# Performance work log

Hardware: AMD Instinct MI355X
Metric: run time of the kernel (lower is better)

The kernel has to match this reference:

```python
import jax, jax.numpy as jnp
import numpy as np

DIM = 256          # model dim
H = 8              # num heads
E = DIM // H       # head dim = 32
M = 32             # ball size
NB = 8192          # number of balls
N = NB * M         # total points = 262144
D3 = 3             # spatial dimensionality


def setup_inputs() -> dict:
    key = jax.random.key(0)
    ks = jax.random.split(key, 10)
    s = 1.0 / np.sqrt(DIM)
    return {
        "x": jax.random.normal(ks[0], (N, DIM), jnp.float32),
        "pos": jax.random.normal(ks[1], (N, D3), jnp.float32),
        "w_qkv": jax.random.normal(ks[2], (DIM, 3 * DIM), jnp.float32) * s,
        "b_qkv": jnp.zeros((3 * DIM,), jnp.float32),
        "w_pe": jax.random.normal(ks[3], (D3, DIM), jnp.float32) * (1.0 / np.sqrt(D3)),
        "b_pe": jnp.zeros((DIM,), jnp.float32),
        "w_proj": jax.random.normal(ks[4], (DIM, DIM), jnp.float32) * s,
        "b_proj": jnp.zeros((DIM,), jnp.float32),
        "sigma_att": -1.0 + 0.01 * jax.random.normal(ks[5], (1, H, 1, 1), jnp.float32),
    }


def reference(x, pos, w_qkv, b_qkv, w_pe, b_pe, w_proj, b_proj, sigma_att):
    n = x.shape[0] // M
    pos_b = pos.reshape(n, M, D3)                       # (n, m, 3)

    # eq. 9: relative position embedding wrt ball center
    centers = pos_b.mean(axis=1, keepdims=True)         # (n, 1, 3)
    rel = (pos_b - centers).reshape(n * M, D3)
    x = x + rel @ w_pe + b_pe                           # (N, DIM)

    # qkv projection; layout '(H E K)' with K fastest
    qkv = (x @ w_qkv + b_qkv).reshape(n, M, H, E, 3)
    q = jnp.transpose(qkv[..., 0], (0, 2, 1, 3))        # (n, H, m, E)
    k = jnp.transpose(qkv[..., 1], (0, 2, 1, 3))
    v = jnp.transpose(qkv[..., 2], (0, 2, 1, 3))

    # eq. 10: distance-based attention bias
    diff = pos_b[:, :, None, :] - pos_b[:, None, :, :]  # (n, m, m, 3)
    d2 = jnp.sum(diff * diff, axis=-1)
    dist = jnp.sqrt(jnp.maximum(d2, 1e-12))             # safe sqrt (grad at 0)
    bias = sigma_att * dist[:, None, :, :]              # (n, H, m, m)

    scale = 1.0 / np.sqrt(E)
    scores = jnp.einsum('nhme,nhke->nhmk', q, k) * scale + bias
    attn = jax.nn.softmax(scores, axis=-1)
    out = jnp.einsum('nhmk,nhke->nhme', attn, v)        # (n, H, m, E)
    out = jnp.transpose(out, (0, 2, 1, 3)).reshape(n * M, DIM)
    return out @ w_proj + b_proj
```

## Files before the change

kernel.cpp:

```cpp
#include <hip/hip_runtime.h>

#define NPTS   262144
#define NBALLS 8192
#define MSZ    32

typedef unsigned short u16;
typedef __attribute__((ext_vector_type(8))) unsigned short u16x8;
typedef __attribute__((ext_vector_type(8))) __bf16 bf16x8;
typedef __attribute__((ext_vector_type(4))) float f32x4;
typedef __attribute__((ext_vector_type(2))) unsigned u32x2;

__device__ inline u16 f2bf(float f) {
    unsigned u = __builtin_bit_cast(unsigned, f);
    u += 0x7fffu + ((u >> 16) & 1u);
    return (u16)(u >> 16);
}

__device__ inline unsigned pk2(float lo, float hi) {
    return (unsigned)f2bf(lo) | ((unsigned)f2bf(hi) << 16);
}

__device__ inline f32x4 mfma16(u16x8 a, u16x8 b, f32x4 c) {
    return __builtin_amdgcn_mfma_f32_16x16x32_bf16(
        __builtin_bit_cast(bf16x8, a), __builtin_bit_cast(bf16x8, b), c, 0, 0, 0);
}

__device__ inline void gload_lds16(const u16* g, u16* l) {
    __builtin_amdgcn_global_load_lds(
        (const __attribute__((address_space(1))) void*)g,
        (__attribute__((address_space(3))) void*)l, 16, 0, 0);
}

__global__ __launch_bounds__(256) void k0_wprep(const float* __restrict__ w_qkv,
                                                const float* __restrict__ b_qkv,
                                                const float* __restrict__ w_proj,
                                                u16* __restrict__ wqkvT2,
                                                u16* __restrict__ wpF,
                                                float* __restrict__ bq2) {
    int idx = blockIdx.x * 256 + threadIdx.x;
    if (idx < 768 * 256) {
        int cp = idx >> 8, r = idx & 255;
        int h = cp / 96, rem = cp % 96, mat = rem >> 5, e = rem & 31;
        int orig = h * 96 + e * 3 + mat;
        wqkvT2[cp * 256 + r] = f2bf(w_qkv[r * 768 + orig]);
        if (r == 0) bq2[cp] = b_qkv[orig];
    } else {
        int tid2 = idx - 768 * 256;
        int lane = tid2 & 63, ch = tid2 >> 6;
        int hk = ch & 7, gct = ch >> 3;
        int r15 = lane & 15, g4 = lane >> 4;
        u16x8 o;
#pragma unroll
        for (int j = 0; j < 8; ++j)
            o[j] = f2bf(w_proj[(size_t)(hk * 32 + g4 * 8 + j) * 256 + gct * 16 + r15]);
        *(u16x8*)&wpF[(size_t)tid2 * 8] = o;
    }
}

__global__ __launch_bounds__(512, 4) void k1_fused(const float* __restrict__ x,
                                                   const float* __restrict__ pos,
                                                   const float* __restrict__ w_pe,
                                                   const float* __restrict__ b_pe,
                                                   const u16* __restrict__ wqkvT2,
                                                   const float* __restrict__ bq2,
                                                   const float* __restrict__ sigma,
                                                   u16* __restrict__ ao) {
    __shared__ __align__(16) u16 Bs2[2][96 * 64];
    __shared__ __align__(16) u16 qkvh[4][3][MSZ][32];
    __shared__ float dist_s[4][MSZ][32];
    __shared__ __align__(16) char upool[10240];

    float* ps_s  = (float*)upool;
    float* ctr_s = ps_s + 384;
    float* rel_s = ctr_s + 12;
    float* wpe_s = rel_s + 384;
    float* bpe_s = wpe_s + 768;
    typedef u16 (*PsT)[MSZ][40];
    PsT P_s = (PsT)upool;

    int id = blockIdx.x;
    int rt = (id >> 3) + (id & 7) * 256;
    int t = threadIdx.x;
    int lane = t & 63, wv = t >> 6;
    int r15 = lane & 15, g4 = lane >> 4;
    int wr = wv >> 1, wc = wv & 1;
    int rowbase = rt * 128;
    const int ball_g = rt * 4 + wr;
    const float scale = 0.17677669529663687f;

    if (t < 384) ps_s[t] = pos[(size_t)rt * 384 + t];
    if (t < 256) bpe_s[t] = b_pe[t];
    for (int i = t; i < 768; i += 512) wpe_s[i] = w_pe[i];
    {
        int c = t, row = c >> 3, sg = c & 7;
        gload_lds16(&wqkvT2[(size_t)row * 256 + (sg ^ (row & 7)) * 8], &Bs2[0][c * 8]);
        if (t < 256) {
            int c2 = 512 + t, row2 = c2 >> 3, sg2 = c2 & 7;
            gload_lds16(&wqkvT2[(size_t)row2 * 256 + (sg2 ^ (row2 & 7)) * 8], &Bs2[0][c2 * 8]);
        }
    }
    __syncthreads();
    if (t < 12) {
        int b = t / 3, m = t % 3;
        float s = 0.f;
#pragma unroll
        for (int j = 0; j < MSZ; ++j) s += ps_s[(b * 32 + j) * 3 + m];
        ctr_s[b * 3 + m] = s * (1.0f / MSZ);
    }
    __syncthreads();
    if (t < 384) {
        int p = t / 3, m = t % 3;
        rel_s[t] = ps_s[t] - ctr_s[(p >> 5) * 3 + m];
    }
    for (int idx2 = t; idx2 < 4096; idx2 += 512) {
        int b = idx2 >> 10, m = (idx2 >> 5) & 31, kk = idx2 & 31;
        float dx = ps_s[(b * 32 + m) * 3 + 0] - ps_s[(b * 32 + kk) * 3 + 0];
        float dy = ps_s[(b * 32 + m) * 3 + 1] - ps_s[(b * 32 + kk) * 3 + 1];
        float dz = ps_s[(b * 32 + m) * 3 + 2] - ps_s[(b * 32 + kk) * 3 + 2];
        dist_s[b][m][kk] = sqrtf(fmaxf(dx * dx + dy * dy + dz * dz, 1e-12f));
    }
    __syncthreads();

    u16* Ast = &qkvh[0][0][0][0];
    u16x8 af[2][8];
#pragma unroll
    for (int kt = 0; kt < 4; ++kt) {
#pragma unroll
        for (int i = 0; i < 2; ++i) {
            int c = i * 512 + t;
            int row = c >> 3, g = c & 7;
            int kk0 = kt * 64 + g * 8;
            float4 xa = *(const float4*)&x[(size_t)(rowbase + row) * 256 + kk0];
            float4 xb = *(const float4*)&x[(size_t)(rowbase + row) * 256 + kk0 + 4];
            float r0 = rel_s[row * 3 + 0], r1 = rel_s[row * 3 + 1], r2 = rel_s[row * 3 + 2];
            u16x8 o;
#pragma unroll
            for (int m = 0; m < 8; ++m) {
                float xv = (m < 4) ? ((const float*)&xa)[m] : ((const float*)&xb)[m - 4];
                float v = fmaf(r0, wpe_s[0 * 256 + kk0 + m],
                          fmaf(r1, wpe_s[1 * 256 + kk0 + m],
                          fmaf(r2, wpe_s[2 * 256 + kk0 + m], xv))) + bpe_s[kk0 + m];
                o[m] = f2bf(v);
            }
            *(u16x8*)&Ast[(row * 8 + (g ^ (row & 7))) * 8] = o;
        }
        __syncthreads();
#pragma unroll
        for (int ks = 0; ks < 2; ++ks)
#pragma unroll
            for (int i = 0; i < 2; ++i) {
                int R = wr * 32 + i * 16 + r15;
                af[i][2 * kt + ks] =
                    *(const u16x8*)&Ast[R * 64 + (((ks * 4 + g4) ^ (R & 7)) * 8)];
            }
        __syncthreads();
    }

    f32x4 acc[3][2];
#pragma unroll
    for (int j = 0; j < 3; ++j)
#pragma unroll
        for (int i = 0; i < 2; ++i) acc[j][i] = (f32x4){0.f, 0.f, 0.f, 0.f};

    for (int hd = 0; hd < 8; ++hd) {
#pragma unroll
        for (int kt = 0; kt < 4; ++kt) {
            int cur = kt & 1;
            if (hd * 4 + kt < 31) {
                int nhd = (kt == 3) ? hd + 1 : hd;
                int nkt = (kt + 1) & 3;
                int c = t, row = c >> 3, sg = c & 7;
                gload_lds16(&wqkvT2[(size_t)(nhd * 96 + row) * 256 + nkt * 64 + (sg ^ (row & 7)) * 8],
                            &Bs2[cur ^ 1][c * 8]);
                if (t < 256) {
                    int c2 = 512 + t, row2 = c2 >> 3, sg2 = c2 & 7;
                    gload_lds16(&wqkvT2[(size_t)(nhd * 96 + row2) * 256 + nkt * 64 + (sg2 ^ (row2 & 7)) * 8],
                                &Bs2[cur ^ 1][c2 * 8]);
                }
            }
#pragma unroll
            for (int ks = 0; ks < 2; ++ks) {
                u16x8 b[3];
#pragma unroll
                for (int j = 0; j < 3; ++j) {
                    int C = wc * 48 + j * 16 + r15;
                    b[j] = *(const u16x8*)&Bs2[cur][C * 64 + (((ks * 4 + g4) ^ (C & 7)) * 8)];
                }
#pragma unroll
                for (int j = 0; j < 3; ++j)
#pragma unroll
                    for (int i = 0; i < 2; ++i)
                        acc[j][i] = mfma16(b[j], af[i][2 * kt + ks], acc[j][i]);
            }
            if (kt == 3) {
#pragma unroll
                for (int j = 0; j < 3; ++j) {
                    int cp0 = wc * 48 + j * 16 + g4 * 4;
                    float4 bias = *(const float4*)&bq2[hd * 96 + cp0];
                    int mat = cp0 >> 5, e0 = cp0 & 31;
#pragma unroll
                    for (int i = 0; i < 2; ++i) {
                        int point = i * 16 + r15;
                        unsigned lo = pk2(acc[j][i][0] + bias.x, acc[j][i][1] + bias.y);
                        unsigned hi = pk2(acc[j][i][2] + bias.z, acc[j][i][3] + bias.w);
                        int ed = (mat == 2) ? (e0 ^ (((point >> 3) & 1) << 4)) : e0;
                        *(u32x2*)&qkvh[wr][mat][point][ed] = (u32x2){lo, hi};
                        acc[j][i] = (f32x4){0.f, 0.f, 0.f, 0.f};
                    }
                }
            }
            __syncthreads();
        }

        float sig = sigma[hd];
        u16x8 aq[2], bk[2];
#pragma unroll
        for (int i = 0; i < 2; ++i) {
            aq[i] = *(const u16x8*)&qkvh[wr][0][i * 16 + r15][g4 * 8];
            bk[i] = *(const u16x8*)&qkvh[wr][1][i * 16 + r15][g4 * 8];
        }
        f32x4 s[2][2];
#pragma unroll
        for (int i = 0; i < 2; ++i)
#pragma unroll
            for (int j = 0; j < 2; ++j)
                s[i][j] = mfma16(aq[i], bk[j], (f32x4){0.f, 0.f, 0.f, 0.f});

#pragma unroll
        for (int i = 0; i < 2; ++i) {
#pragma unroll
            for (int r = 0; r < 4; ++r) {
                int row = i * 16 + g4 * 4 + r;
                float v0 = s[i][0][r] * scale + sig * dist_s[wr][row][r15];
                float v1 = s[i][1][r] * scale + sig * dist_s[wr][row][16 + r15];
                float m = fmaxf(v0, v1);
                m = fmaxf(m, __shfl_xor(m, 1));
                m = fmaxf(m, __shfl_xor(m, 2));
                m = fmaxf(m, __shfl_xor(m, 4));
                m = fmaxf(m, __shfl_xor(m, 8));
                float e0 = __expf(v0 - m), e1 = __expf(v1 - m);
                float su = e0 + e1;
                su += __shfl_xor(su, 1);
                su += __shfl_xor(su, 2);
                su += __shfl_xor(su, 4);
                su += __shfl_xor(su, 8);
                float rin = 1.0f / su;
                if (wc == 0) {
                    P_s[wr][row][r15]      = f2bf(e0 * rin);
                    P_s[wr][row][16 + r15] = f2bf(e1 * rin);
                }
            }
        }
        __syncthreads();

        u16x8 pa[2];
#pragma unroll
        for (int i = 0; i < 2; ++i)
            pa[i] = *(const u16x8*)&P_s[wr][i * 16 + r15][g4 * 8];
        u16x8 bv;
#pragma unroll
        for (int jj = 0; jj < 8; ++jj) {
            int kp = g4 * 8 + jj;
            int ev = (wc * 16 + r15) ^ (((kp >> 3) & 1) << 4);
            bv[jj] = qkvh[wr][2][kp][ev];
        }
#pragma unroll
        for (int i = 0; i < 2; ++i) {
            f32x4 o = mfma16(bv, pa[i], (f32x4){0.f, 0.f, 0.f, 0.f});
            int point = i * 16 + r15;
            int e0 = wc * 16 + g4 * 4;
            unsigned lo = pk2(o[0], o[1]);
            unsigned hi = pk2(o[2], o[3]);
            *(u32x2*)&ao[(size_t)(ball_g * 32 + point) * 256 + hd * 32 + e0] = (u32x2){lo, hi};
        }
        __syncthreads();
    }
}

__global__ __launch_bounds__(256) void k2_proj(const u16* __restrict__ ao,
                                               const u16* __restrict__ wpF,
                                               const float* __restrict__ bp,
                                               float* __restrict__ out) {
    int ball = blockIdx.x, t = threadIdx.x;
    int lane = t & 63, wv = t >> 6;
    int r15 = lane & 15, g4 = lane >> 4;
    const size_t rowb = (size_t)ball * 32;

    f32x4 pacc[4][2];
#pragma unroll
    for (int tt = 0; tt < 4; ++tt)
#pragma unroll
        for (int i = 0; i < 2; ++i) pacc[tt][i] = (f32x4){0.f, 0.f, 0.f, 0.f};
#pragma unroll
    for (int hk = 0; hk < 8; ++hk) {
        u16x8 apj[2];
#pragma unroll
        for (int i = 0; i < 2; ++i)
            apj[i] = *(const u16x8*)&ao[(rowb + i * 16 + r15) * 256 + hk * 32 + g4 * 8];
#pragma unroll
        for (int tt = 0; tt < 4; ++tt) {
            int gct = wv * 4 + tt;
            u16x8 b = *(const u16x8*)&wpF[(size_t)((gct * 8 + hk) * 64 + lane) * 8];
            pacc[tt][0] = mfma16(apj[0], b, pacc[tt][0]);
            pacc[tt][1] = mfma16(apj[1], b, pacc[tt][1]);
        }
    }
#pragma unroll
    for (int tt = 0; tt < 4; ++tt) {
        int ct = (wv * 4 + tt) * 16;
        float bb = bp[ct + r15];
#pragma unroll
        for (int i = 0; i < 2; ++i)
#pragma unroll
            for (int r = 0; r < 4; ++r) {
                size_t row = rowb + i * 16 + g4 * 4 + r;
                out[row * 256 + ct + r15] = pacc[tt][i][r] + bb;
            }
    }
}

extern "C" void kernel_launch(void* const* d_in, const int* in_sizes, int n_in,
                              void* d_out, int out_size, void* d_ws, size_t ws_size,
                              hipStream_t stream) {
    (void)in_sizes; (void)n_in; (void)out_size; (void)ws_size;
    const float* x      = (const float*)d_in[0];
    const float* pos    = (const float*)d_in[1];
    const float* w_qkv  = (const float*)d_in[2];
    const float* b_qkv  = (const float*)d_in[3];
    const float* w_pe   = (const float*)d_in[4];
    const float* b_pe   = (const float*)d_in[5];
    const float* w_proj = (const float*)d_in[6];
    const float* b_proj = (const float*)d_in[7];
    const float* sigma  = (const float*)d_in[8];
    float* out = (float*)d_out;

    u16* ao      = (u16*)d_ws;
    u16* wqkvT2  = ao + (size_t)NPTS * 256;
    u16* wpF     = wqkvT2 + 768 * 256;
    float* bq2   = (float*)(wpF + 65536);

    k0_wprep<<<800, 256, 0, stream>>>(w_qkv, b_qkv, w_proj, wqkvT2, wpF, bq2);
    k1_fused<<<2048, 512, 0, stream>>>(x, pos, w_pe, b_pe, wqkvT2, bq2, sigma, ao);
    k2_proj<<<NBALLS, 256, 0, stream>>>(ao, wpF, b_proj, out);
}
```

Before: 520.4 us.

## Load QKV weights directly from global in MFMA fragment layout, dropping LDS staging

```diff
diff --git a/kernel.cpp b/kernel.cpp
--- a/kernel.cpp
+++ b/kernel.cpp
@@ -25,27 +25,32 @@
         __builtin_bit_cast(bf16x8, a), __builtin_bit_cast(bf16x8, b), c, 0, 0, 0);
 }
 
-__device__ inline void gload_lds16(const u16* g, u16* l) {
-    __builtin_amdgcn_global_load_lds(
-        (const __attribute__((address_space(1))) void*)g,
-        (__attribute__((address_space(3))) void*)l, 16, 0, 0);
-}
-
 __global__ __launch_bounds__(256) void k0_wprep(const float* __restrict__ w_qkv,
                                                 const float* __restrict__ b_qkv,
                                                 const float* __restrict__ w_proj,
-                                                u16* __restrict__ wqkvT2,
+                                                u16* __restrict__ wqkvF,
                                                 u16* __restrict__ wpF,
                                                 float* __restrict__ bq2) {
-    int idx = blockIdx.x * 256 + threadIdx.x;
-    if (idx < 768 * 256) {
-        int cp = idx >> 8, r = idx & 255;
+    int g = blockIdx.x * 256 + threadIdx.x;
+    if (g < 768) {
+        int cp = g;
+        int h = cp / 96, rem = cp % 96, mat = rem >> 5, e = rem & 31;
+        bq2[cp] = b_qkv[h * 96 + e * 3 + mat];
+    }
+    if (g < 24576) {
+        int lane = g & 63, ks = (g >> 6) & 7, tile = g >> 9;
+        int r15 = lane & 15, g4 = lane >> 4;
+        int cp = tile * 16 + r15;
         int h = cp / 96, rem = cp % 96, mat = rem >> 5, e = rem & 31;
         int orig = h * 96 + e * 3 + mat;
-        wqkvT2[cp * 256 + r] = f2bf(w_qkv[r * 768 + orig]);
-        if (r == 0) bq2[cp] = b_qkv[orig];
+        int k0 = ks * 32 + g4 * 8;
+        u16x8 o;
+#pragma unroll
+        for (int j = 0; j < 8; ++j)
+            o[j] = f2bf(w_qkv[(size_t)(k0 + j) * 768 + orig]);
+        *(u16x8*)&wqkvF[(size_t)g * 8] = o;
     } else {
-        int tid2 = idx - 768 * 256;
+        int tid2 = g - 24576;
         int lane = tid2 & 63, ch = tid2 >> 6;
         int hk = ch & 7, gct = ch >> 3;
         int r15 = lane & 15, g4 = lane >> 4;
@@ -61,13 +66,12 @@
                                                    const float* __restrict__ pos,
                                                    const float* __restrict__ w_pe,
                                                    const float* __restrict__ b_pe,
-                                                   const u16* __restrict__ wqkvT2,
+                                                   const u16* __restrict__ wqkvF,
                                                    const float* __restrict__ bq2,
                                                    const float* __restrict__ sigma,
                                                    u16* __restrict__ ao) {
-    __shared__ __align__(16) u16 Bs2[2][96 * 64];
-    __shared__ __align__(16) u16 qkvh[4][3][MSZ][32];
-    __shared__ float dist_s[4][MSZ][32];
+    __shared__ __align__(16) u16 qkvh[4][3][MSZ][40];
+    __shared__ float dist_s[4][MSZ][33];
     __shared__ __align__(16) char upool[10240];
 
     float* ps_s  = (float*)upool;
@@ -91,14 +95,6 @@
     if (t < 384) ps_s[t] = pos[(size_t)rt * 384 + t];
     if (t < 256) bpe_s[t] = b_pe[t];
     for (int i = t; i < 768; i += 512) wpe_s[i] = w_pe[i];
-    {
-        int c = t, row = c >> 3, sg = c & 7;
-        gload_lds16(&wqkvT2[(size_t)row * 256 + (sg ^ (row & 7)) * 8], &Bs2[0][c * 8]);
-        if (t < 256) {
-            int c2 = 512 + t, row2 = c2 >> 3, sg2 = c2 & 7;
-            gload_lds16(&wqkvT2[(size_t)row2 * 256 + (sg2 ^ (row2 & 7)) * 8], &Bs2[0][c2 * 8]);
-        }
-    }
     __syncthreads();
     if (t < 12) {
         int b = t / 3, m = t % 3;
@@ -156,61 +152,42 @@
         __syncthreads();
     }
 
-    f32x4 acc[3][2];
-#pragma unroll
-    for (int j = 0; j < 3; ++j)
-#pragma unroll
-        for (int i = 0; i < 2; ++i) acc[j][i] = (f32x4){0.f, 0.f, 0.f, 0.f};
-
     for (int hd = 0; hd < 8; ++hd) {
-#pragma unroll
-        for (int kt = 0; kt < 4; ++kt) {
-            int cur = kt & 1;
-            if (hd * 4 + kt < 31) {
-                int nhd = (kt == 3) ? hd + 1 : hd;
-                int nkt = (kt + 1) & 3;
-                int c = t, row = c >> 3, sg = c & 7;
-                gload_lds16(&wqkvT2[(size_t)(nhd * 96 + row) * 256 + nkt * 64 + (sg ^ (row & 7)) * 8],
-                            &Bs2[cur ^ 1][c * 8]);
-                if (t < 256) {
-                    int c2 = 512 + t, row2 = c2 >> 3, sg2 = c2 & 7;
-                    gload_lds16(&wqkvT2[(size_t)(nhd * 96 + row2) * 256 + nkt * 64 + (sg2 ^ (row2 & 7)) * 8],
-                                &Bs2[cur ^ 1][c2 * 8]);
-                }
-            }
-#pragma unroll
-            for (int ks = 0; ks < 2; ++ks) {
-                u16x8 b[3];
-#pragma unroll
-                for (int j = 0; j < 3; ++j) {
-                    int C = wc * 48 + j * 16 + r15;
-                    b[j] = *(const u16x8*)&Bs2[cur][C * 64 + (((ks * 4 + g4) ^ (C & 7)) * 8)];
-                }
-#pragma unroll
-                for (int j = 0; j < 3; ++j)
-#pragma unroll
-                    for (int i = 0; i < 2; ++i)
-                        acc[j][i] = mfma16(b[j], af[i][2 * kt + ks], acc[j][i]);
-            }
-            if (kt == 3) {
-#pragma unroll
-                for (int j = 0; j < 3; ++j) {
-                    int cp0 = wc * 48 + j * 16 + g4 * 4;
-                    float4 bias = *(const float4*)&bq2[hd * 96 + cp0];
-                    int mat = cp0 >> 5, e0 = cp0 & 31;
-#pragma unroll
-                    for (int i = 0; i < 2; ++i) {
-                        int point = i * 16 + r15;
-                        unsigned lo = pk2(acc[j][i][0] + bias.x, acc[j][i][1] + bias.y);
-                        unsigned hi = pk2(acc[j][i][2] + bias.z, acc[j][i][3] + bias.w);
-                        int ed = (mat == 2) ? (e0 ^ (((point >> 3) & 1) << 4)) : e0;
-                        *(u32x2*)&qkvh[wr][mat][point][ed] = (u32x2){lo, hi};
-                        acc[j][i] = (f32x4){0.f, 0.f, 0.f, 0.f};
-                    }
-                }
-            }
-            __syncthreads();
-        }
+        f32x4 acc[3][2];
+#pragma unroll
+        for (int j = 0; j < 3; ++j)
+#pragma unroll
+            for (int i = 0; i < 2; ++i) acc[j][i] = (f32x4){0.f, 0.f, 0.f, 0.f};
+
+#pragma unroll
+        for (int ks = 0; ks < 8; ++ks) {
+            u16x8 b[3];
+#pragma unroll
+            for (int j = 0; j < 3; ++j) {
+                int tile = hd * 6 + wc * 3 + j;
+                b[j] = *(const u16x8*)&wqkvF[(size_t)((tile * 8 + ks) * 64 + lane) * 8];
+            }
+#pragma unroll
+            for (int j = 0; j < 3; ++j)
+#pragma unroll
+                for (int i = 0; i < 2; ++i)
+                    acc[j][i] = mfma16(b[j], af[i][ks], acc[j][i]);
+        }
+#pragma unroll
+        for (int j = 0; j < 3; ++j) {
+            int cp0 = wc * 48 + j * 16 + g4 * 4;
+            float4 bias = *(const float4*)&bq2[hd * 96 + cp0];
+            int mat = cp0 >> 5, e0 = cp0 & 31;
+#pragma unroll
+            for (int i = 0; i < 2; ++i) {
+                int point = i * 16 + r15;
+                unsigned lo = pk2(acc[j][i][0] + bias.x, acc[j][i][1] + bias.y);
+                unsigned hi = pk2(acc[j][i][2] + bias.z, acc[j][i][3] + bias.w);
+                int ed = (mat == 2) ? (e0 ^ (((point >> 3) & 1) << 4)) : e0;
+                *(u32x2*)&qkvh[wr][mat][point][ed] = (u32x2){lo, hi};
+            }
+        }
+        __syncthreads();
 
         float sig = sigma[hd];
         u16x8 aq[2], bk[2];
@@ -334,12 +311,12 @@
     const float* sigma  = (const float*)d_in[8];
     float* out = (float*)d_out;
 
-    u16* ao      = (u16*)d_ws;
-    u16* wqkvT2  = ao + (size_t)NPTS * 256;
-    u16* wpF     = wqkvT2 + 768 * 256;
-    float* bq2   = (float*)(wpF + 65536);
-
-    k0_wprep<<<800, 256, 0, stream>>>(w_qkv, b_qkv, w_proj, wqkvT2, wpF, bq2);
-    k1_fused<<<2048, 512, 0, stream>>>(x, pos, w_pe, b_pe, wqkvT2, bq2, sigma, ao);
+    u16* ao     = (u16*)d_ws;
+    u16* wqkvF  = ao + (size_t)NPTS * 256;
+    u16* wpF    = wqkvF + 196608;
+    float* bq2  = (float*)(wpF + 65536);
+
+    k0_wprep<<<128, 256, 0, stream>>>(w_qkv, b_qkv, w_proj, wqkvF, wpF, bq2);
+    k1_fused<<<2048, 512, 0, stream>>>(x, pos, w_pe, b_pe, wqkvF, bq2, sigma, ao);
     k2_proj<<<NBALLS, 256, 0, stream>>>(ao, wpF, b_proj, out);
 }
```

Result: faster. 504.8 us, median of 2 (-3.0%).
